# Optimization experiments

Measured on AMD Instinct MI355X. Metric: run time of the kernel, lower is better.

Reference implementation:

```python
import jax, jax.numpy as jnp
import numpy as np

D_MODEL = 2048
NHEAD = 32
N_KV = 8
HEAD_DIM = D_MODEL // NHEAD
EPS = 1e-5


def setup_inputs() -> dict:
    key = jax.random.key(0)
    k1, k2, k3, k4, k5 = jax.random.split(key, 5)
    B, S = 2, 2048
    return {
        "x": jax.random.normal(k1, (B, S, D_MODEL), dtype=jnp.float32),
        "wq": jax.random.normal(k2, (D_MODEL, D_MODEL), dtype=jnp.float32) * 0.02,
        "wk": jax.random.normal(k3, (N_KV * HEAD_DIM, D_MODEL), dtype=jnp.float32) * 0.02,
        "wv": jax.random.normal(k4, (N_KV * HEAD_DIM, D_MODEL), dtype=jnp.float32) * 0.02,
        "wo": jax.random.normal(k5, (D_MODEL, D_MODEL), dtype=jnp.float32) * 0.02,
    }


def weight_quant(w):
    # ternary/binary quant with straight-through estimator
    scale = jnp.maximum(jnp.mean(jnp.abs(w)), EPS)
    return jax.lax.stop_gradient(jnp.sign(w) * scale - w) + w


def bitlinear(x, w):
    # F.linear(x, weight_quant(w)) = x @ w_q.T
    return x @ weight_quant(w).T


def reference(x, wq, wk, wv, wo):
    B, S, _ = x.shape
    G = NHEAD // N_KV  # kv groups
    # projections
    q = bitlinear(x, wq).reshape(B, S, N_KV, G, HEAD_DIM)   # [B,S,Kv,G,D]
    k = bitlinear(x, wk).reshape(B, S, N_KV, HEAD_DIM)      # [B,S,Kv,D]
    v = bitlinear(x, wv).reshape(B, S, N_KV, HEAD_DIM)
    # GQA causal attention without materializing repeated K/V
    sm_scale = 1.0 / jnp.sqrt(jnp.asarray(HEAD_DIM, dtype=x.dtype))
    scores = jnp.einsum('bskgd,btkd->bkgst', q, k) * sm_scale  # [B,Kv,G,S,S]
    causal = jnp.tril(jnp.ones((S, S), dtype=bool))
    scores = jnp.where(causal, scores, jnp.asarray(-jnp.inf, dtype=scores.dtype))
    probs = jax.nn.softmax(scores, axis=-1)
    out = jnp.einsum('bkgst,btkd->bskgd', probs, v)  # [B,S,Kv,G,D]
    out = out.reshape(B, S, D_MODEL)
    return bitlinear(out, wo)
```

## Files before the change

### kernel.cpp

```cpp
#include <hip/hip_runtime.h>
#include <stdint.h>


#define D_MODEL 2048
#define S_LEN   2048
#define BATCH   2
#define NKV     8
#define HD      64
#define MROWS   (BATCH * S_LEN)
#define NQKV    3072
#define LDQKV   3072

typedef unsigned short u16;
typedef __bf16 bf16x8 __attribute__((ext_vector_type(8)));
typedef float  f32x4  __attribute__((ext_vector_type(4)));
typedef float  f32x16 __attribute__((ext_vector_type(16)));
typedef unsigned u32x4 __attribute__((ext_vector_type(4)));

__device__ __forceinline__ u16 f2bf(float f) {
  union { float f; unsigned u; } v; v.f = f;
  unsigned r = v.u + 0x7FFFu + ((v.u >> 16) & 1u);
  return (u16)(r >> 16);
}

__device__ __forceinline__ float exp2_fast(float x) {
  float r; asm("v_exp_f32 %0, %1" : "=v"(r) : "v"(x)); return r;
}

__device__ __forceinline__ unsigned cvt_pk_bf16(float a, float b) {
  unsigned r;
  asm("v_cvt_pk_bf16_f32 %0, %1, %2" : "=v"(r) : "v"(a), "v"(b));
  return r;
}

__device__ __forceinline__ void lds_load16(u16* lds, const u16* g) {
  __builtin_amdgcn_global_load_lds(
      (const __attribute__((address_space(1))) void*)g,
      (__attribute__((address_space(3))) void*)lds, 16, 0, 0);
}

#define SM_LOG2E 0.180336880f
#define THR_LOG2 11.5415603f

__global__ void prep_all(const float* __restrict__ wq, const float* __restrict__ wk,
                         const float* __restrict__ wv, const float* __restrict__ wo,
                         const float* __restrict__ x,
                         u16* __restrict__ wqkvs, u16* __restrict__ wos,
                         u16* __restrict__ xb, double* __restrict__ partials) {
  const int bid = blockIdx.x;
  const float* src; u16* dst; int n4, rb, nb; bool sgn = true;
  if (bid < 256)      { src = wq; dst = wqkvs;                  n4 = 1048576; rb = bid;       nb = 256; }
  else if (bid < 320) { src = wk; dst = wqkvs + 2048 * D_MODEL; n4 = 262144;  rb = bid - 256; nb = 64;  }
  else if (bid < 384) { src = wv; dst = wqkvs + 2560 * D_MODEL; n4 = 262144;  rb = bid - 320; nb = 64;  }
  else if (bid < 640) { src = wo; dst = wos;                    n4 = 1048576; rb = bid - 384; nb = 256; }
  else                { src = x;  dst = xb;                     n4 = 2097152; rb = bid - 640; nb = 512; sgn = false; }

  if (sgn) {
    double s = 0.0;
    for (int i = rb * 256 + threadIdx.x; i < n4; i += nb * 256) {
      float4 v = reinterpret_cast<const float4*>(src)[i];
      ushort4 o;
      o.x = v.x > 0.f ? 0x3F80 : (v.x < 0.f ? 0xBF80 : 0);
      o.y = v.y > 0.f ? 0x3F80 : (v.y < 0.f ? 0xBF80 : 0);
      o.z = v.z > 0.f ? 0x3F80 : (v.z < 0.f ? 0xBF80 : 0);
      o.w = v.w > 0.f ? 0x3F80 : (v.w < 0.f ? 0xBF80 : 0);
      reinterpret_cast<ushort4*>(dst)[i] = o;
      s += (double)fabsf(v.x) + (double)fabsf(v.y) +
           (double)fabsf(v.z) + (double)fabsf(v.w);
    }
    __shared__ double sm[256];
    sm[threadIdx.x] = s;
    __syncthreads();
    for (int off = 128; off > 0; off >>= 1) {
      if (threadIdx.x < off) sm[threadIdx.x] += sm[threadIdx.x + off];
      __syncthreads();
    }
    if (threadIdx.x == 0) partials[bid] = sm[0];
  } else {
    for (int i = rb * 256 + threadIdx.x; i < n4; i += nb * 256) {
      float4 v = reinterpret_cast<const float4*>(src)[i];
      ushort4 o;
      o.x = f2bf(v.x); o.y = f2bf(v.y); o.z = f2bf(v.z); o.w = f2bf(v.w);
      reinterpret_cast<ushort4*>(dst)[i] = o;
    }
  }
}

__global__ void finalize_scales(const double* __restrict__ partials,
                                float* __restrict__ tabs) {
  __shared__ float sc_sh[4];
  const int w = threadIdx.x >> 6;
  const int lane = threadIdx.x & 63;
  const int beg[4] = {0, 256, 320, 384};
  const int cnt[4] = {256, 64, 64, 256};
  const double counts[4] = {4194304.0, 1048576.0, 1048576.0, 4194304.0};
  double s = 0.0;
  for (int i = lane; i < cnt[w]; i += 64) s += partials[beg[w] + i];
  for (int off = 1; off < 64; off <<= 1) s += __shfl_xor(s, off);
  if (lane == 0) sc_sh[w] = fmaxf((float)(s / counts[w]), 1e-5f);
  __syncthreads();
  if (threadIdx.x == 0) {
    tabs[0] = sc_sh[0] * SM_LOG2E;
    tabs[1] = sc_sh[1];
    tabs[2] = sc_sh[2];
    tabs[3] = sc_sh[3];
  }
}

template <int BN, int OUT_BF16, int QKVMODE>
__global__ __launch_bounds__(512, 4) void gemm_dp(
    const u16* __restrict__ A, const u16* __restrict__ Bt, void* __restrict__ Cv,
    const float* __restrict__ tabs4, u16* __restrict__ vt, int M, int N, int K) {
  constexpr int WN = BN / 4;
  constexpr int NFR = WN / 16;
  constexpr int BITER = BN / 64;
  constexpr int STEADY = 2 + BITER;
  __shared__ u16 lA[2][128 * 64];
  __shared__ u16 lB[2][BN * 64];
  const int tid = threadIdx.x;
  const int lane = tid & 63, wave = tid >> 6;
  const int lo = lane & 15, hi = lane >> 4;
  const int m0 = blockIdx.y * 128, n0 = blockIdx.x * BN;
  const int wr = (wave >> 2) * 64;
  const int wc = (wave & 3) * WN;
  const int swl = (lo & 7) << 3;

  f32x4 acc[4][NFR] = {};
  const int nt = K >> 6;

  auto STAGE = [&](int bf, int kt) {
    const int k0s = kt * 64;
#pragma unroll
    for (int it = 0; it < 2; ++it) {
      const int c = it * 512 + tid;
      const int row = c >> 3;
      const int ch = (c & 7) ^ (row & 7);
      lds_load16(&lA[bf][(it * 512 + wave * 64) * 8],
                 &A[(size_t)(m0 + row) * K + k0s + ch * 8]);
    }
#pragma unroll
    for (int it = 0; it < BITER; ++it) {
      const int c = it * 512 + tid;
      const int row = c >> 3;
      const int ch = (c & 7) ^ (row & 7);
      lds_load16(&lB[bf][(it * 512 + wave * 64) * 8],
                 &Bt[(size_t)(n0 + row) * K + k0s + ch * 8]);
    }
  };

  STAGE(0, 0);
  STAGE(1, 1);

#pragma unroll 1
  for (int kt = 0; kt < nt; ++kt) {
    const int cur = kt & 1;
    if (kt + 1 < nt) {
      if constexpr (BITER == 3)
        asm volatile("s_waitcnt vmcnt(5)\n\ts_barrier" ::: "memory");
      else
        asm volatile("s_waitcnt vmcnt(4)\n\ts_barrier" ::: "memory");
    } else {
      asm volatile("s_waitcnt vmcnt(0)\n\ts_barrier" ::: "memory");
    }
    __builtin_amdgcn_sched_barrier(0);

    const u16* la = lA[cur];
    const u16* lb = lB[cur];
#pragma unroll
    for (int kk = 0; kk < 2; ++kk) {
      bf16x8 af[4], bfr[NFR];
#pragma unroll
      for (int i = 0; i < 4; ++i)
        af[i] = *reinterpret_cast<const bf16x8*>(
            &la[(wr + i * 16 + lo) * 64 + ((kk * 32 + hi * 8) ^ swl)]);
#pragma unroll
      for (int i = 0; i < NFR; ++i)
        bfr[i] = *reinterpret_cast<const bf16x8*>(
            &lb[(wc + i * 16 + lo) * 64 + ((kk * 32 + hi * 8) ^ swl)]);
      __builtin_amdgcn_s_setprio(1);
#pragma unroll
      for (int mi = 0; mi < 4; ++mi)
#pragma unroll
        for (int ni = 0; ni < NFR; ++ni)
          acc[mi][ni] = __builtin_amdgcn_mfma_f32_16x16x32_bf16(
              af[mi], bfr[ni], acc[mi][ni], 0, 0, 0);
      __builtin_amdgcn_s_setprio(0);
    }
    __builtin_amdgcn_sched_barrier(0);
    asm volatile("s_barrier" ::: "memory");
    if (kt + 2 < nt) STAGE(cur, kt + 2);
  }

  const float s0 = tabs4[0];
#pragma unroll
  for (int mi = 0; mi < 4; ++mi) {
#pragma unroll
    for (int ni = 0; ni < NFR; ++ni) {
      const int col0 = n0 + wc + ni * 16;
      float scale = s0;
      if (QKVMODE) scale = col0 < 2048 ? s0 : (col0 < 2560 ? tabs4[1] : tabs4[2]);
      if (QKVMODE && col0 >= 2560) {
        const int vcol = col0 - 2560 + lo;
        const int row = m0 + wr + mi * 16 + hi * 4;
        unsigned w01 = cvt_pk_bf16(acc[mi][ni][0] * scale, acc[mi][ni][1] * scale);
        unsigned w23 = cvt_pk_bf16(acc[mi][ni][2] * scale, acc[mi][ni][3] * scale);
        uint2 pk; pk.x = w01; pk.y = w23;
        *reinterpret_cast<uint2*>(vt + (size_t)vcol * MROWS + row) = pk;
      } else {
#pragma unroll
        for (int r = 0; r < 4; ++r) {
          const int row = m0 + wr + mi * 16 + hi * 4 + r;
          const int col = col0 + lo;
          const float v = acc[mi][ni][r] * scale;
          if (OUT_BF16)
            reinterpret_cast<u16*>(Cv)[(size_t)row * N + col] = f2bf(v);
          else
            reinterpret_cast<float*>(Cv)[(size_t)row * N + col] = v;
        }
      }
    }
  }
}

__device__ __forceinline__ void stage_tile(u16* dst, const u16* base, int ld,
                                           int tid, int wave) {
#pragma unroll
  for (int it = 0; it < 2; ++it) {
    const int c = it * 256 + tid;
    const int row = c >> 3;
    const int ch = (c & 7) ^ (row & 7);
    lds_load16(dst + (it * 256 + wave * 64) * 8, base + (size_t)row * ld + ch * 8);
  }
}

#define TILE_BODY(MASKED)                                                      \
  {                                                                            \
    const int t0 = ti * 64;                                                    \
    const int cur = ti & 1;                                                    \
    u16* lKc = (u16*)lK[cur];                                                  \
    u16* lVc = (u16*)lV[cur];                                                  \
    f32x16 sacc[2] = {};                                                       \
    __builtin_amdgcn_s_setprio(1);                                             \
    _Pragma("unroll")                                                          \
    for (int w = 0; w < 4; ++w) {                                              \
      _Pragma("unroll")                                                        \
      for (int nf = 0; nf < 2; ++nf) {                                         \
        bf16x8 kf = *reinterpret_cast<const bf16x8*>(                          \
            &lKc[(nf * 32 + q31) * 64 + ((w * 16 + hi5 * 8) ^ swl)]);          \
        sacc[nf] = __builtin_amdgcn_mfma_f32_32x32x16_bf16(                    \
            kf, qf[w], sacc[nf], 0, 0, 0);                                     \
      }                                                                        \
    }                                                                          \
    __builtin_amdgcn_s_setprio(0);                                             \
    if (ti + 1 < nt) {                                                         \
      stage_tile(lK[cur ^ 1], Kb + (size_t)(brow + t0 + 64) * LDQKV, LDQKV,    \
                 tid, wave);                                                   \
      stage_tile(lV[cur ^ 1], Vb + t0 + 64, MROWS, tid, wave);                 \
    }                                                                          \
    if (MASKED) {                                                              \
      _Pragma("unroll")                                                        \
      for (int nf = 0; nf < 2; ++nf) {                                         \
        _Pragma("unroll")                                                      \
        for (int rg = 0; rg < 16; ++rg) {                                      \
          const int tg = t0 + nf * 32 + (rg >> 2) * 8 + hi5 * 4 + (rg & 3);    \
          if (tg > qg) sacc[nf][rg] = -1e30f;                                  \
        }                                                                      \
      }                                                                        \
    }                                                                          \
    float mt = -1e30f;                                                         \
    _Pragma("unroll")                                                          \
    for (int nf = 0; nf < 2; ++nf) {                                           \
      _Pragma("unroll")                                                        \
      for (int rg = 0; rg < 16; ++rg) mt = fmaxf(mt, sacc[nf][rg]);            \
    }                                                                          \
    mt = fmaxf(mt, __shfl_xor(mt, 32));                                        \
    if (!__all((int)(mt <= m_run + THR_LOG2))) {                               \
      const float mn = fmaxf(m_run, mt);                                       \
      const float alpha = exp2_fast(m_run - mn);                               \
      m_run = mn;                                                              \
      l_lane *= alpha;                                                         \
      _Pragma("unroll")                                                        \
      for (int nf = 0; nf < 2; ++nf) {                                         \
        _Pragma("unroll")                                                      \
        for (int rg = 0; rg < 16; ++rg) oacc[nf][rg] *= alpha;                 \
      }                                                                        \
    }                                                                          \
    unsigned pk[2][8];                                                         \
    _Pragma("unroll")                                                          \
    for (int nf = 0; nf < 2; ++nf) {                                           \
      _Pragma("unroll")                                                        \
      for (int c = 0; c < 4; ++c) {                                            \
        const float e0 = exp2_fast(sacc[nf][4 * c + 0] - m_run);               \
        const float e1 = exp2_fast(sacc[nf][4 * c + 1] - m_run);               \
        const float e2 = exp2_fast(sacc[nf][4 * c + 2] - m_run);               \
        const float e3 = exp2_fast(sacc[nf][4 * c + 3] - m_run);               \
        l_lane += (e0 + e1) + (e2 + e3);                                       \
        pk[nf][2 * c + 0] = cvt_pk_bf16(e0, e1);                               \
        pk[nf][2 * c + 1] = cvt_pk_bf16(e2, e3);                               \
      }                                                                        \
    }                                                                          \
    __builtin_amdgcn_s_setprio(1);                                             \
    _Pragma("unroll")                                                          \
    for (int w = 0; w < 4; ++w) {                                              \
      const int nf = w >> 1, c4 = (w & 1) * 4;                                 \
      unsigned a0 = pk[nf][c4 + 0], a1 = pk[nf][c4 + 1];                       \
      unsigned b0 = pk[nf][c4 + 2], b1 = pk[nf][c4 + 3];                       \
      asm volatile("v_permlane32_swap_b32 %0, %1" : "+v"(a0), "+v"(b0));       \
      asm volatile("v_permlane32_swap_b32 %0, %1" : "+v"(a1), "+v"(b1));       \
      u32x4 pw; pw.x = a0; pw.y = a1; pw.z = b0; pw.w = b1;                    \
      bf16x8 pfr = *reinterpret_cast<const bf16x8*>(&pw);                      \
      _Pragma("unroll")                                                        \
      for (int nfo = 0; nfo < 2; ++nfo) {                                      \
        bf16x8 vf = *reinterpret_cast<const bf16x8*>(                          \
            &lVc[(nfo * 32 + q31) * 64 + ((w * 16 + hi5 * 8) ^ swl)]);         \
        oacc[nfo] = __builtin_amdgcn_mfma_f32_32x32x16_bf16(                   \
            vf, pfr, oacc[nfo], 0, 0, 0);                                      \
      }                                                                        \
    }                                                                          \
    __builtin_amdgcn_s_setprio(0);                                             \
    __syncthreads();                                                           \
  }

__global__ __launch_bounds__(256, 2) void flash_attn(
    const u16* __restrict__ QKV, const u16* __restrict__ VT,
    u16* __restrict__ Og) {
  __shared__ u16 lK[2][64 * 64];
  __shared__ u16 lV[2][64 * 64];

  const int tid = threadIdx.x;
  const int lane = tid & 63, wave = tid >> 6;
  const int q31 = lane & 31, hi5 = lane >> 5;
  const int lin = (int)blockIdx.y * 8 + (int)blockIdx.x;
  const int xcd = lin & 7, slot = lin >> 3;
  const int G = xcd * 2 + (slot >> 5);
  const int wb = slot & 31;
  const int b = G >> 3, kv = G & 7;
  const int h = kv * 4 + (wb >> 3);
  const int lbx = wb & 7;
  const int brow = b * S_LEN;
  const u16* Q  = QKV + h * HD;
  const u16* Kb = QKV + 2048 + kv * HD;
  const u16* Vb = VT + (size_t)(kv * HD) * MROWS + brow;
  const int swl = (lane & 7) << 3;

#pragma unroll 1
  for (int pi = 0; pi < 2; ++pi) {
    const int qt = pi == 0 ? lbx : (15 - lbx);
    const int q0 = qt * 128;
    const int q0w = q0 + wave * 32;
    const int nt = 2 * qt + 2;
    const int qg = q0w + q31;

    bf16x8 qf[4];
    {
      const size_t qr = (size_t)(brow + q0w + q31) * LDQKV;
#pragma unroll
      for (int w = 0; w < 4; ++w)
        qf[w] = *reinterpret_cast<const bf16x8*>(&Q[qr + w * 16 + hi5 * 8]);
    }

    f32x16 oacc[2] = {};
    float m_run = -1e30f, l_lane = 0.f;

    stage_tile(lK[0], Kb + (size_t)brow * LDQKV, LDQKV, tid, wave);
    stage_tile(lV[0], Vb, MROWS, tid, wave);
    __syncthreads();

#pragma unroll 1
    for (int ti = 0; ti < 2 * qt; ++ti) TILE_BODY(0)
#pragma unroll 1
    for (int ti = 2 * qt; ti < nt; ++ti) TILE_BODY(1)

    {
      float ls = l_lane;
      ls += __shfl_xor(ls, 32);
      const float inv = 1.f / ls;
#pragma unroll
      for (int nfo = 0; nfo < 2; ++nfo) {
#pragma unroll
        for (int c = 0; c < 4; ++c) {
          const unsigned u0 = cvt_pk_bf16(oacc[nfo][4 * c + 0] * inv,
                                          oacc[nfo][4 * c + 1] * inv);
          const unsigned u1 = cvt_pk_bf16(oacc[nfo][4 * c + 2] * inv,
                                          oacc[nfo][4 * c + 3] * inv);
          const int d = nfo * 32 + c * 8 + hi5 * 4;
          uint2 st; st.x = u0; st.y = u1;
          *reinterpret_cast<uint2*>(
              &Og[(size_t)(brow + q0w + q31) * D_MODEL + h * HD + d]) = st;
        }
      }
    }
  }
}

extern "C" void kernel_launch(void* const* d_in, const int* in_sizes, int n_in,
                              void* d_out, int out_size, void* d_ws, size_t ws_size,
                              hipStream_t stream) {
  (void)in_sizes; (void)n_in; (void)out_size; (void)ws_size;
  const float* x  = (const float*)d_in[0];
  const float* wq = (const float*)d_in[1];
  const float* wk = (const float*)d_in[2];
  const float* wv = (const float*)d_in[3];
  const float* wo = (const float*)d_in[4];
  float* out = (float*)d_out;
  char* ws = (char*)d_ws;

  double* partials = (double*)ws;
  float* tabs = (float*)(ws + 6144);
  size_t off = 8192;
  u16* xb    = (u16*)(ws + off); off += (size_t)MROWS * D_MODEL * 2;
  u16* wqkvs = (u16*)(ws + off); off += (size_t)NQKV * D_MODEL * 2;
  u16* wos   = (u16*)(ws + off); off += (size_t)D_MODEL * D_MODEL * 2;
  u16* qkvb  = (u16*)(ws + off); off += (size_t)MROWS * NQKV * 2;
  u16* ao    = (u16*)(ws + off); off += (size_t)MROWS * D_MODEL * 2;
  u16* vt    = (u16*)(ws + off); off += (size_t)512 * MROWS * 2;

  prep_all<<<1152, 256, 0, stream>>>(wq, wk, wv, wo, x, wqkvs, wos, xb, partials);
  finalize_scales<<<1, 256, 0, stream>>>(partials, tabs);

  gemm_dp<192, 1, 1><<<dim3(NQKV / 192, MROWS / 128), 512, 0, stream>>>(
      xb, wqkvs, qkvb, tabs, vt, MROWS, NQKV, D_MODEL);

  flash_attn<<<dim3(8, 64), 256, 0, stream>>>(qkvb, vt, ao);

  gemm_dp<128, 0, 0><<<dim3(D_MODEL / 128, MROWS / 128), 512, 0, stream>>>(
      ao, wos, out, tabs + 3, nullptr, MROWS, D_MODEL, D_MODEL);
}
```

Baseline: 158.6 us.

## Split long causal attention rows across two blocks with split-KV merge

Doubles the flash-attention grid so each block pair shares work evenly. One block computes a short query tile fully plus the first half of a long tile's KV range, and the other block computes the rest. The two partial results are written unnormalized in bf16 with row max and sum, then combined by a new merge kernel. Occupancy is raised to 4 blocks per CU and the xb buffer is reused as scratch. This adds a kernel launch, extra global traffic and bf16 rounding of the partial outputs.

New measurement: 166.9 us. 1.05x slower.

```diff
diff --git a/kernel.cpp b/kernel.cpp
--- a/kernel.cpp
+++ b/kernel.cpp
@@ -21,6 +21,10 @@
   union { float f; unsigned u; } v; v.f = f;
   unsigned r = v.u + 0x7FFFu + ((v.u >> 16) & 1u);
   return (u16)(r >> 16);
+}
+
+__device__ __forceinline__ float bf2f(u16 u) {
+  union { unsigned u; float f; } v; v.u = ((unsigned)u) << 16; return v.f;
 }
 
 __device__ __forceinline__ float exp2_fast(float x) {
@@ -114,7 +118,6 @@
   constexpr int WN = BN / 4;
   constexpr int NFR = WN / 16;
   constexpr int BITER = BN / 64;
-  constexpr int STEADY = 2 + BITER;
   __shared__ u16 lA[2][128 * 64];
   __shared__ u16 lB[2][BN * 64];
   const int tid = threadIdx.x;
@@ -233,10 +236,9 @@
   }
 }
 
-#define TILE_BODY(MASKED)                                                      \
+#define TILE_BODY(MASKED, TEND)                                                \
   {                                                                            \
     const int t0 = ti * 64;                                                    \
-    const int cur = ti & 1;                                                    \
     u16* lKc = (u16*)lK[cur];                                                  \
     u16* lVc = (u16*)lV[cur];                                                  \
     f32x16 sacc[2] = {};                                                       \
@@ -252,7 +254,7 @@
       }                                                                        \
     }                                                                          \
     __builtin_amdgcn_s_setprio(0);                                             \
-    if (ti + 1 < nt) {                                                         \
+    if (ti + 1 < (TEND)) {                                                     \
       stage_tile(lK[cur ^ 1], Kb + (size_t)(brow + t0 + 64) * LDQKV, LDQKV,    \
                  tid, wave);                                                   \
       stage_tile(lV[cur ^ 1], Vb + t0 + 64, MROWS, tid, wave);                 \
@@ -319,58 +321,65 @@
     }                                                                          \
     __builtin_amdgcn_s_setprio(0);                                             \
     __syncthreads();                                                           \
-  }
-
-__global__ __launch_bounds__(256, 2) void flash_attn(
+    cur ^= 1;                                                                  \
+  }
+
+#define INIT_PASS(QT)                                                          \
+  {                                                                            \
+    qt = (QT); q0 = qt * 128; q0w = q0 + wave * 32; qg = q0w + q31;            \
+    const size_t qr = (size_t)(brow + q0w + q31) * LDQKV;                      \
+    _Pragma("unroll")                                                          \
+    for (int w = 0; w < 4; ++w)                                                \
+      qf[w] = *reinterpret_cast<const bf16x8*>(&Q[qr + w * 16 + hi5 * 8]);     \
+    _Pragma("unroll")                                                          \
+    for (int z = 0; z < 16; ++z) { oacc[0][z] = 0.f; oacc[1][z] = 0.f; }       \
+    m_run = -1e30f; l_lane = 0.f;                                              \
+  }
+
+#define RUN_TILES(TBEG, MBEG, TEND)                                            \
+  {                                                                            \
+    cur = 0;                                                                   \
+    stage_tile(lK[0], Kb + (size_t)(brow + (TBEG) * 64) * LDQKV, LDQKV, tid,   \
+               wave);                                                          \
+    stage_tile(lV[0], Vb + (TBEG) * 64, MROWS, tid, wave);                     \
+    __syncthreads();                                                           \
+    _Pragma("unroll 1")                                                        \
+    for (int ti = (TBEG); ti < (MBEG); ++ti) TILE_BODY(0, TEND)                \
+    _Pragma("unroll 1")                                                        \
+    for (int ti = (MBEG); ti < (TEND); ++ti) TILE_BODY(1, TEND)                \
+  }
+
+__global__ __launch_bounds__(256, 4) void flash_attn(
     const u16* __restrict__ QKV, const u16* __restrict__ VT,
-    u16* __restrict__ Og) {
+    u16* __restrict__ Og, u16* __restrict__ part, float2* __restrict__ ml) {
   __shared__ u16 lK[2][64 * 64];
   __shared__ u16 lV[2][64 * 64];
 
   const int tid = threadIdx.x;
   const int lane = tid & 63, wave = tid >> 6;
   const int q31 = lane & 31, hi5 = lane >> 5;
-  const int lin = (int)blockIdx.y * 8 + (int)blockIdx.x;
+  const int lin = (int)blockIdx.y * 16 + (int)blockIdx.x;
   const int xcd = lin & 7, slot = lin >> 3;
-  const int G = xcd * 2 + (slot >> 5);
-  const int wb = slot & 31;
+  const int G = xcd * 2 + (slot >> 6);
+  const int rest = slot & 63;
   const int b = G >> 3, kv = G & 7;
-  const int h = kv * 4 + (wb >> 3);
-  const int lbx = wb & 7;
+  const int h = kv * 4 + (rest >> 4);
+  const int p = rest & 15;
+  const int ipair = p >> 1, half = p & 1;
   const int brow = b * S_LEN;
   const u16* Q  = QKV + h * HD;
   const u16* Kb = QKV + 2048 + kv * HD;
   const u16* Vb = VT + (size_t)(kv * HD) * MROWS + brow;
   const int swl = (lane & 7) << 3;
 
-#pragma unroll 1
-  for (int pi = 0; pi < 2; ++pi) {
-    const int qt = pi == 0 ? lbx : (15 - lbx);
-    const int q0 = qt * 128;
-    const int q0w = q0 + wave * 32;
-    const int nt = 2 * qt + 2;
-    const int qg = q0w + q31;
-
-    bf16x8 qf[4];
-    {
-      const size_t qr = (size_t)(brow + q0w + q31) * LDQKV;
-#pragma unroll
-      for (int w = 0; w < 4; ++w)
-        qf[w] = *reinterpret_cast<const bf16x8*>(&Q[qr + w * 16 + hi5 * 8]);
-    }
-
-    f32x16 oacc[2] = {};
-    float m_run = -1e30f, l_lane = 0.f;
-
-    stage_tile(lK[0], Kb + (size_t)brow * LDQKV, LDQKV, tid, wave);
-    stage_tile(lV[0], Vb, MROWS, tid, wave);
-    __syncthreads();
-
-#pragma unroll 1
-    for (int ti = 0; ti < 2 * qt; ++ti) TILE_BODY(0)
-#pragma unroll 1
-    for (int ti = 2 * qt; ti < nt; ++ti) TILE_BODY(1)
-
+  int qt, q0, q0w, qg, cur;
+  bf16x8 qf[4];
+  f32x16 oacc[2];
+  float m_run, l_lane;
+
+  if (half == 0) {
+    INIT_PASS(ipair)
+    RUN_TILES(0, 2 * qt, 2 * qt + 2)
     {
       float ls = l_lane;
       ls += __shfl_xor(ls, 32);
@@ -390,7 +399,75 @@
         }
       }
     }
-  }
+    INIT_PASS(15 - ipair)
+    RUN_TILES(0, 15 - 2 * ipair, 15 - 2 * ipair)
+    {
+      const float lt = l_lane + __shfl_xor(l_lane, 32);
+      const int prow = b * 1024 + (q0w + q31 - 1024);
+#pragma unroll
+      for (int nfo = 0; nfo < 2; ++nfo) {
+#pragma unroll
+        for (int c = 0; c < 4; ++c) {
+          const unsigned u0 = cvt_pk_bf16(oacc[nfo][4 * c + 0], oacc[nfo][4 * c + 1]);
+          const unsigned u1 = cvt_pk_bf16(oacc[nfo][4 * c + 2], oacc[nfo][4 * c + 3]);
+          const int d = nfo * 32 + c * 8 + hi5 * 4;
+          uint2 st; st.x = u0; st.y = u1;
+          *reinterpret_cast<uint2*>(&part[(size_t)prow * 2048 + h * HD + d]) = st;
+        }
+      }
+      if (lane < 32) { float2 v; v.x = m_run; v.y = lt; ml[prow * 32 + h] = v; }
+    }
+  } else {
+    INIT_PASS(15 - ipair)
+    RUN_TILES(15 - 2 * ipair, 30 - 2 * ipair, 32 - 2 * ipair)
+    {
+      const float lt = l_lane + __shfl_xor(l_lane, 32);
+      const int prow = b * 1024 + (q0w + q31 - 1024);
+#pragma unroll
+      for (int nfo = 0; nfo < 2; ++nfo) {
+#pragma unroll
+        for (int c = 0; c < 4; ++c) {
+          const unsigned u0 = cvt_pk_bf16(oacc[nfo][4 * c + 0], oacc[nfo][4 * c + 1]);
+          const unsigned u1 = cvt_pk_bf16(oacc[nfo][4 * c + 2], oacc[nfo][4 * c + 3]);
+          const int d = nfo * 32 + c * 8 + hi5 * 4;
+          uint2 st; st.x = u0; st.y = u1;
+          *reinterpret_cast<uint2*>(
+              &part[(size_t)(2048 * 2048) + (size_t)prow * 2048 + h * HD + d]) = st;
+        }
+      }
+      if (lane < 32) { float2 v; v.x = m_run; v.y = lt; ml[(2048 + prow) * 32 + h] = v; }
+    }
+  }
+}
+
+__global__ __launch_bounds__(256) void merge_halves(
+    const u16* __restrict__ part, const float2* __restrict__ ml,
+    u16* __restrict__ ao) {
+  const int idx = blockIdx.x * 256 + threadIdx.x;
+  const int prow = idx >> 8;
+  const int col = (idx & 255) * 8;
+  const int h = col >> 6;
+  const float2 a = ml[prow * 32 + h];
+  const float2 c = ml[(2048 + prow) * 32 + h];
+  const float M = fmaxf(a.x, c.x);
+  const float e0 = exp2_fast(a.x - M), e1 = exp2_fast(c.x - M);
+  const float inv = 1.f / (a.y * e0 + c.y * e1);
+  const float s0 = e0 * inv, s1 = e1 * inv;
+  const uint4 p0 = *reinterpret_cast<const uint4*>(&part[(size_t)prow * 2048 + col]);
+  const uint4 p1 = *reinterpret_cast<const uint4*>(
+      &part[(size_t)(2048 * 2048) + (size_t)prow * 2048 + col]);
+  const unsigned* w0 = reinterpret_cast<const unsigned*>(&p0);
+  const unsigned* w1 = reinterpret_cast<const unsigned*>(&p1);
+  uint4 o;
+  unsigned* ow = reinterpret_cast<unsigned*>(&o);
+#pragma unroll
+  for (int j = 0; j < 4; ++j) {
+    const float x0 = bf2f((u16)(w0[j] & 0xffffu)) * s0 + bf2f((u16)(w1[j] & 0xffffu)) * s1;
+    const float x1 = bf2f((u16)(w0[j] >> 16)) * s0 + bf2f((u16)(w1[j] >> 16)) * s1;
+    ow[j] = cvt_pk_bf16(x0, x1);
+  }
+  const int grow = (prow >> 10) * S_LEN + 1024 + (prow & 1023);
+  *reinterpret_cast<uint4*>(&ao[(size_t)grow * D_MODEL + col]) = o;
 }
 
 extern "C" void kernel_launch(void* const* d_in, const int* in_sizes, int n_in,
@@ -414,6 +491,7 @@
   u16* qkvb  = (u16*)(ws + off); off += (size_t)MROWS * NQKV * 2;
   u16* ao    = (u16*)(ws + off); off += (size_t)MROWS * D_MODEL * 2;
   u16* vt    = (u16*)(ws + off); off += (size_t)512 * MROWS * 2;
+  float2* ml = (float2*)(ws + off); off += (size_t)2 * 2048 * 32 * 8;
 
   prep_all<<<1152, 256, 0, stream>>>(wq, wk, wv, wo, x, wqkvs, wos, xb, partials);
   finalize_scales<<<1, 256, 0, stream>>>(partials, tabs);
@@ -421,7 +499,9 @@
   gemm_dp<192, 1, 1><<<dim3(NQKV / 192, MROWS / 128), 512, 0, stream>>>(
       xb, wqkvs, qkvb, tabs, vt, MROWS, NQKV, D_MODEL);
 
-  flash_attn<<<dim3(8, 64), 256, 0, stream>>>(qkvb, vt, ao);
+  flash_attn<<<dim3(16, 64), 256, 0, stream>>>(qkvb, vt, ao, xb, ml);
+
+  merge_halves<<<2048, 256, 0, stream>>>(xb, ml, ao);
 
   gemm_dp<128, 0, 0><<<dim3(D_MODEL / 128, MROWS / 128), 512, 0, stream>>>(
       ao, wos, out, tabs + 3, nullptr, MROWS, D_MODEL, D_MODEL);
```

## Process both paired causal query tiles in one pass sharing K/V tiles

Applied to the files above, without the earlier changes.

The flash attention kernel used to handle its two query tiles (a short one and its mirrored long one) one after the other, loading K/V from the start for each. It now runs a single loop over the long tile's range. Each staged K/V tile feeds both query tiles while the short one is still active, which removes the duplicate K/V staging and barriers for the shared prefix. In exchange each thread holds two sets of Q fragments, accumulators and softmax state, which raises register pressure and could hurt occupancy or cause spills.

Result: slower. 168.4 us (+6.2%).

```diff
diff --git a/kernel.cpp b/kernel.cpp
--- a/kernel.cpp
+++ b/kernel.cpp
@@ -114,7 +114,6 @@
   constexpr int WN = BN / 4;
   constexpr int NFR = WN / 16;
   constexpr int BITER = BN / 64;
-  constexpr int STEADY = 2 + BITER;
   __shared__ u16 lA[2][128 * 64];
   __shared__ u16 lB[2][BN * 64];
   const int tid = threadIdx.x;
@@ -233,37 +232,15 @@
   }
 }
 
-#define TILE_BODY(MASKED)                                                      \
+#define SM_CTX(SACC, MRUN, LRUN, OACC, QG, NTX, PK)                            \
   {                                                                            \
-    const int t0 = ti * 64;                                                    \
-    const int cur = ti & 1;                                                    \
-    u16* lKc = (u16*)lK[cur];                                                  \
-    u16* lVc = (u16*)lV[cur];                                                  \
-    f32x16 sacc[2] = {};                                                       \
-    __builtin_amdgcn_s_setprio(1);                                             \
-    _Pragma("unroll")                                                          \
-    for (int w = 0; w < 4; ++w) {                                              \
-      _Pragma("unroll")                                                        \
-      for (int nf = 0; nf < 2; ++nf) {                                         \
-        bf16x8 kf = *reinterpret_cast<const bf16x8*>(                          \
-            &lKc[(nf * 32 + q31) * 64 + ((w * 16 + hi5 * 8) ^ swl)]);          \
-        sacc[nf] = __builtin_amdgcn_mfma_f32_32x32x16_bf16(                    \
-            kf, qf[w], sacc[nf], 0, 0, 0);                                     \
-      }                                                                        \
-    }                                                                          \
-    __builtin_amdgcn_s_setprio(0);                                             \
-    if (ti + 1 < nt) {                                                         \
-      stage_tile(lK[cur ^ 1], Kb + (size_t)(brow + t0 + 64) * LDQKV, LDQKV,    \
-                 tid, wave);                                                   \
-      stage_tile(lV[cur ^ 1], Vb + t0 + 64, MROWS, tid, wave);                 \
-    }                                                                          \
-    if (MASKED) {                                                              \
+    if (ti >= (NTX) - 2) {                                                     \
       _Pragma("unroll")                                                        \
       for (int nf = 0; nf < 2; ++nf) {                                         \
         _Pragma("unroll")                                                      \
         for (int rg = 0; rg < 16; ++rg) {                                      \
           const int tg = t0 + nf * 32 + (rg >> 2) * 8 + hi5 * 4 + (rg & 3);    \
-          if (tg > qg) sacc[nf][rg] = -1e30f;                                  \
+          if (tg > (QG)) SACC[nf][rg] = -1e30f;                                \
         }                                                                      \
       }                                                                        \
     }                                                                          \
@@ -271,54 +248,65 @@
     _Pragma("unroll")                                                          \
     for (int nf = 0; nf < 2; ++nf) {                                           \
       _Pragma("unroll")                                                        \
-      for (int rg = 0; rg < 16; ++rg) mt = fmaxf(mt, sacc[nf][rg]);            \
+      for (int rg = 0; rg < 16; ++rg) mt = fmaxf(mt, SACC[nf][rg]);            \
     }                                                                          \
     mt = fmaxf(mt, __shfl_xor(mt, 32));                                        \
-    if (!__all((int)(mt <= m_run + THR_LOG2))) {                               \
-      const float mn = fmaxf(m_run, mt);                                       \
-      const float alpha = exp2_fast(m_run - mn);                               \
-      m_run = mn;                                                              \
-      l_lane *= alpha;                                                         \
+    if (!__all((int)(mt <= MRUN + THR_LOG2))) {                                \
+      const float mn = fmaxf(MRUN, mt);                                        \
+      const float alpha = exp2_fast(MRUN - mn);                                \
+      MRUN = mn;                                                               \
+      LRUN *= alpha;                                                           \
       _Pragma("unroll")                                                        \
       for (int nf = 0; nf < 2; ++nf) {                                         \
         _Pragma("unroll")                                                      \
-        for (int rg = 0; rg < 16; ++rg) oacc[nf][rg] *= alpha;                 \
+        for (int rg = 0; rg < 16; ++rg) OACC[nf][rg] *= alpha;                 \
       }                                                                        \
     }                                                                          \
-    unsigned pk[2][8];                                                         \
     _Pragma("unroll")                                                          \
     for (int nf = 0; nf < 2; ++nf) {                                           \
       _Pragma("unroll")                                                        \
       for (int c = 0; c < 4; ++c) {                                            \
-        const float e0 = exp2_fast(sacc[nf][4 * c + 0] - m_run);               \
-        const float e1 = exp2_fast(sacc[nf][4 * c + 1] - m_run);               \
-        const float e2 = exp2_fast(sacc[nf][4 * c + 2] - m_run);               \
-        const float e3 = exp2_fast(sacc[nf][4 * c + 3] - m_run);               \
-        l_lane += (e0 + e1) + (e2 + e3);                                       \
-        pk[nf][2 * c + 0] = cvt_pk_bf16(e0, e1);                               \
-        pk[nf][2 * c + 1] = cvt_pk_bf16(e2, e3);                               \
+        const float e0 = exp2_fast(SACC[nf][4 * c + 0] - MRUN);                \
+        const float e1 = exp2_fast(SACC[nf][4 * c + 1] - MRUN);                \
+        const float e2 = exp2_fast(SACC[nf][4 * c + 2] - MRUN);                \
+        const float e3 = exp2_fast(SACC[nf][4 * c + 3] - MRUN);                \
+        LRUN += (e0 + e1) + (e2 + e3);                                         \
+        PK[nf][2 * c + 0] = cvt_pk_bf16(e0, e1);                               \
+        PK[nf][2 * c + 1] = cvt_pk_bf16(e2, e3);                               \
       }                                                                        \
     }                                                                          \
-    __builtin_amdgcn_s_setprio(1);                                             \
+  }
+
+#define PFR(PK, W, OUT)                                                        \
+  bf16x8 OUT;                                                                  \
+  {                                                                            \
+    const int nf_ = (W) >> 1, c4_ = ((W) & 1) * 4;                             \
+    unsigned a0 = PK[nf_][c4_ + 0], a1 = PK[nf_][c4_ + 1];                     \
+    unsigned b0 = PK[nf_][c4_ + 2], b1 = PK[nf_][c4_ + 3];                     \
+    asm volatile("v_permlane32_swap_b32 %0, %1" : "+v"(a0), "+v"(b0));         \
+    asm volatile("v_permlane32_swap_b32 %0, %1" : "+v"(a1), "+v"(b1));         \
+    u32x4 pw; pw.x = a0; pw.y = a1; pw.z = b0; pw.w = b1;                      \
+    OUT = *reinterpret_cast<const bf16x8*>(&pw);                               \
+  }
+
+#define EPILOGUE(OACC, LRUN, Q0W)                                              \
+  {                                                                            \
+    const float ls = LRUN + __shfl_xor(LRUN, 32);                              \
+    const float inv = 1.f / ls;                                                \
     _Pragma("unroll")                                                          \
-    for (int w = 0; w < 4; ++w) {                                              \
-      const int nf = w >> 1, c4 = (w & 1) * 4;                                 \
-      unsigned a0 = pk[nf][c4 + 0], a1 = pk[nf][c4 + 1];                       \
-      unsigned b0 = pk[nf][c4 + 2], b1 = pk[nf][c4 + 3];                       \
-      asm volatile("v_permlane32_swap_b32 %0, %1" : "+v"(a0), "+v"(b0));       \
-      asm volatile("v_permlane32_swap_b32 %0, %1" : "+v"(a1), "+v"(b1));       \
-      u32x4 pw; pw.x = a0; pw.y = a1; pw.z = b0; pw.w = b1;                    \
-      bf16x8 pfr = *reinterpret_cast<const bf16x8*>(&pw);                      \
+    for (int nfo = 0; nfo < 2; ++nfo) {                                        \
       _Pragma("unroll")                                                        \
-      for (int nfo = 0; nfo < 2; ++nfo) {                                      \
-        bf16x8 vf = *reinterpret_cast<const bf16x8*>(                          \
-            &lVc[(nfo * 32 + q31) * 64 + ((w * 16 + hi5 * 8) ^ swl)]);         \
-        oacc[nfo] = __builtin_amdgcn_mfma_f32_32x32x16_bf16(                   \
-            vf, pfr, oacc[nfo], 0, 0, 0);                                      \
+      for (int c = 0; c < 4; ++c) {                                            \
+        const unsigned u0 = cvt_pk_bf16(OACC[nfo][4 * c + 0] * inv,            \
+                                        OACC[nfo][4 * c + 1] * inv);           \
+        const unsigned u1 = cvt_pk_bf16(OACC[nfo][4 * c + 2] * inv,            \
+                                        OACC[nfo][4 * c + 3] * inv);           \
+        const int d = nfo * 32 + c * 8 + hi5 * 4;                              \
+        uint2 st; st.x = u0; st.y = u1;                                        \
+        *reinterpret_cast<uint2*>(                                             \
+            &Og[(size_t)(brow + (Q0W) + q31) * D_MODEL + h * HD + d]) = st;    \
       }                                                                        \
     }                                                                          \
-    __builtin_amdgcn_s_setprio(0);                                             \
-    __syncthreads();                                                           \
   }
 
 __global__ __launch_bounds__(256, 2) void flash_attn(
@@ -343,54 +331,106 @@
   const u16* Vb = VT + (size_t)(kv * HD) * MROWS + brow;
   const int swl = (lane & 7) << 3;
 
+  const int ntA = 2 * lbx + 2;
+  const int ntB = 32 - 2 * lbx;
+  const int q0wA = lbx * 128 + wave * 32;
+  const int q0wB = (15 - lbx) * 128 + wave * 32;
+  const int qgA = q0wA + q31, qgB = q0wB + q31;
+
+  bf16x8 qfA[4], qfB[4];
+  {
+    const size_t qrA = (size_t)(brow + q0wA + q31) * LDQKV;
+    const size_t qrB = (size_t)(brow + q0wB + q31) * LDQKV;
+#pragma unroll
+    for (int w = 0; w < 4; ++w) {
+      qfA[w] = *reinterpret_cast<const bf16x8*>(&Q[qrA + w * 16 + hi5 * 8]);
+      qfB[w] = *reinterpret_cast<const bf16x8*>(&Q[qrB + w * 16 + hi5 * 8]);
+    }
+  }
+
+  f32x16 oA[2] = {}, oB[2] = {};
+  float mA = -1e30f, lA_ = 0.f, mB = -1e30f, lB_ = 0.f;
+  int cur = 0;
+
+  stage_tile(lK[0], Kb + (size_t)brow * LDQKV, LDQKV, tid, wave);
+  stage_tile(lV[0], Vb, MROWS, tid, wave);
+  __syncthreads();
+
 #pragma unroll 1
-  for (int pi = 0; pi < 2; ++pi) {
-    const int qt = pi == 0 ? lbx : (15 - lbx);
-    const int q0 = qt * 128;
-    const int q0w = q0 + wave * 32;
-    const int nt = 2 * qt + 2;
-    const int qg = q0w + q31;
-
-    bf16x8 qf[4];
-    {
-      const size_t qr = (size_t)(brow + q0w + q31) * LDQKV;
-#pragma unroll
-      for (int w = 0; w < 4; ++w)
-        qf[w] = *reinterpret_cast<const bf16x8*>(&Q[qr + w * 16 + hi5 * 8]);
-    }
-
-    f32x16 oacc[2] = {};
-    float m_run = -1e30f, l_lane = 0.f;
-
-    stage_tile(lK[0], Kb + (size_t)brow * LDQKV, LDQKV, tid, wave);
-    stage_tile(lV[0], Vb, MROWS, tid, wave);
-    __syncthreads();
-
-#pragma unroll 1
-    for (int ti = 0; ti < 2 * qt; ++ti) TILE_BODY(0)
-#pragma unroll 1
-    for (int ti = 2 * qt; ti < nt; ++ti) TILE_BODY(1)
-
-    {
-      float ls = l_lane;
-      ls += __shfl_xor(ls, 32);
-      const float inv = 1.f / ls;
-#pragma unroll
-      for (int nfo = 0; nfo < 2; ++nfo) {
-#pragma unroll
-        for (int c = 0; c < 4; ++c) {
-          const unsigned u0 = cvt_pk_bf16(oacc[nfo][4 * c + 0] * inv,
-                                          oacc[nfo][4 * c + 1] * inv);
-          const unsigned u1 = cvt_pk_bf16(oacc[nfo][4 * c + 2] * inv,
-                                          oacc[nfo][4 * c + 3] * inv);
-          const int d = nfo * 32 + c * 8 + hi5 * 4;
-          uint2 st; st.x = u0; st.y = u1;
-          *reinterpret_cast<uint2*>(
-              &Og[(size_t)(brow + q0w + q31) * D_MODEL + h * HD + d]) = st;
+  for (int ti = 0; ti < ntB; ++ti) {
+    const int t0 = ti * 64;
+    u16* lKc = (u16*)lK[cur];
+    u16* lVc = (u16*)lV[cur];
+    const bool actA = ti < ntA;
+
+    f32x16 sA[2] = {}, sB[2] = {};
+    __builtin_amdgcn_s_setprio(1);
+    if (actA) {
+#pragma unroll
+      for (int w = 0; w < 4; ++w) {
+#pragma unroll
+        for (int nf = 0; nf < 2; ++nf) {
+          bf16x8 kf = *reinterpret_cast<const bf16x8*>(
+              &lKc[(nf * 32 + q31) * 64 + ((w * 16 + hi5 * 8) ^ swl)]);
+          sA[nf] = __builtin_amdgcn_mfma_f32_32x32x16_bf16(kf, qfA[w], sA[nf], 0, 0, 0);
+          sB[nf] = __builtin_amdgcn_mfma_f32_32x32x16_bf16(kf, qfB[w], sB[nf], 0, 0, 0);
         }
       }
-    }
-  }
+    } else {
+#pragma unroll
+      for (int w = 0; w < 4; ++w) {
+#pragma unroll
+        for (int nf = 0; nf < 2; ++nf) {
+          bf16x8 kf = *reinterpret_cast<const bf16x8*>(
+              &lKc[(nf * 32 + q31) * 64 + ((w * 16 + hi5 * 8) ^ swl)]);
+          sB[nf] = __builtin_amdgcn_mfma_f32_32x32x16_bf16(kf, qfB[w], sB[nf], 0, 0, 0);
+        }
+      }
+    }
+    __builtin_amdgcn_s_setprio(0);
+
+    if (ti + 1 < ntB) {
+      stage_tile(lK[cur ^ 1], Kb + (size_t)(brow + t0 + 64) * LDQKV, LDQKV, tid, wave);
+      stage_tile(lV[cur ^ 1], Vb + t0 + 64, MROWS, tid, wave);
+    }
+
+    unsigned pkA[2][8], pkB[2][8];
+    if (actA) SM_CTX(sA, mA, lA_, oA, qgA, ntA, pkA)
+    SM_CTX(sB, mB, lB_, oB, qgB, ntB, pkB)
+
+    __builtin_amdgcn_s_setprio(1);
+    if (actA) {
+#pragma unroll
+      for (int w = 0; w < 4; ++w) {
+        PFR(pkA, w, pfA)
+        PFR(pkB, w, pfB)
+#pragma unroll
+        for (int nfo = 0; nfo < 2; ++nfo) {
+          bf16x8 vf = *reinterpret_cast<const bf16x8*>(
+              &lVc[(nfo * 32 + q31) * 64 + ((w * 16 + hi5 * 8) ^ swl)]);
+          oA[nfo] = __builtin_amdgcn_mfma_f32_32x32x16_bf16(vf, pfA, oA[nfo], 0, 0, 0);
+          oB[nfo] = __builtin_amdgcn_mfma_f32_32x32x16_bf16(vf, pfB, oB[nfo], 0, 0, 0);
+        }
+      }
+    } else {
+#pragma unroll
+      for (int w = 0; w < 4; ++w) {
+        PFR(pkB, w, pfB)
+#pragma unroll
+        for (int nfo = 0; nfo < 2; ++nfo) {
+          bf16x8 vf = *reinterpret_cast<const bf16x8*>(
+              &lVc[(nfo * 32 + q31) * 64 + ((w * 16 + hi5 * 8) ^ swl)]);
+          oB[nfo] = __builtin_amdgcn_mfma_f32_32x32x16_bf16(vf, pfB, oB[nfo], 0, 0, 0);
+        }
+      }
+    }
+    __builtin_amdgcn_s_setprio(0);
+    __syncthreads();
+    cur ^= 1;
+  }
+
+  EPILOGUE(oA, lA_, q0wA)
+  EPILOGUE(oB, lB_, q0wB)
 }
 
 extern "C" void kernel_launch(void* const* d_in, const int* in_sizes, int n_in,
```
